# Kernel optimization log

Measured on AMD Instinct MI355X. Metric: run time of the kernel, lower is better.

## Reference

```python
import jax, jax.numpy as jnp
import numpy as np


def setup_inputs() -> dict:
    key = jax.random.key(0)
    ks = jax.random.split(key, 8)
    B, N = 4, 256
    E, C, H = 64, 128, 256
    return {
        "edge_features": jax.random.normal(ks[0], (B, E, N, N), dtype=jnp.float32),
        "node_features": jax.random.normal(ks[1], (B, C, N), dtype=jnp.float32),
        "W1": jax.random.normal(ks[2], (H, E + 2 * C), dtype=jnp.float32) * 0.05,
        "b1": jax.random.normal(ks[3], (H,), dtype=jnp.float32) * 0.05,
        "W2": jax.random.normal(ks[4], (H, H), dtype=jnp.float32) * 0.05,
        "b2": jax.random.normal(ks[5], (H,), dtype=jnp.float32) * 0.05,
        "W3": jax.random.normal(ks[6], (1, H), dtype=jnp.float32) * 0.05,
        "b3": jax.random.normal(ks[7], (1,), dtype=jnp.float32) * 0.05,
    }


def reference(edge_features, node_features, W1, b1, W2, b2, W3, b3):
    B, C, N = node_features.shape
    # node_addon_row: [B, C, N, N] broadcast along last dim; col along dim 2
    row = jnp.broadcast_to(node_features[:, :, :, None], (B, C, N, N))
    col = jnp.broadcast_to(node_features[:, :, None, :], (B, C, N, N))
    x = jnp.concatenate([edge_features, row, col], axis=1)  # [B, E+2C, N, N]
    # 1x1 conv == channel matmul
    x = jax.nn.relu(jnp.einsum('bcnm,oc->bonm', x, W1) + b1[None, :, None, None])
    x = jax.nn.relu(jnp.einsum('bcnm,oc->bonm', x, W2) + b2[None, :, None, None])
    x = jnp.einsum('bcnm,oc->bonm', x, W3) + b3[None, :, None, None]  # [B,1,N,N]
    return x[:, 0, :, :]
```

## Files before the change

kernel.cpp:

```cpp
#include <hip/hip_runtime.h>
#include <stdint.h>

typedef __bf16 bf16x8 __attribute__((ext_vector_type(8)));
typedef __bf16 bf16x4v __attribute__((ext_vector_type(4)));
typedef float  f32x16 __attribute__((ext_vector_type(16)));
typedef float  f32x4t __attribute__((ext_vector_type(4)));
typedef unsigned int u32x2 __attribute__((ext_vector_type(2)));

#define WS_W1S 0
#define WS_W2S 32768
#define WS_R   163840
#define WS_CT  1212416

__global__ __launch_bounds__(256) void prep_all(
    const float* __restrict__ W1, const float* __restrict__ b1,
    const float* __restrict__ W2, const float* __restrict__ node,
    const float* __restrict__ b3, __bf16* __restrict__ w1s,
    __bf16* __restrict__ w2s, float* __restrict__ Rt,
    __bf16* __restrict__ Ctb, float* __restrict__ out) {
    __shared__ float nds[128 * 8];
    const int blk = blockIdx.x;
    if (blk >= 168) {
        float v = b3[0];
        float4 f4 = make_float4(v, v, v, v);
        *(float4*)(out + (blk - 168) * 1024 + threadIdx.x * 4) = f4;
        return;
    }
    if (blk < 40) {
        int t = blk * 256 + threadIdx.x;
        int chunk = t >> 6, lane = t & 63;
        if (chunk < 128) {
            int wid = chunk >> 5, ks = (chunk >> 1) & 15, mb = chunk & 1;
            int o = wid * 64 + mb * 32 + (lane & 31);
            int k = ks * 16 + (lane >> 5) * 8;
            const float* src = W2 + o * 256 + k;
            __bf16* dst = w2s + chunk * 512 + lane * 8;
#pragma unroll
            for (int j = 0; j < 8; ++j) dst[j] = (__bf16)src[j];
        } else if (chunk < 160) {
            int c1 = chunk - 128;
            int wid = c1 >> 3, ks = (c1 >> 1) & 3, mb = c1 & 1;
            int o = wid * 64 + mb * 32 + (lane & 31);
            int k = ks * 16 + (lane >> 5) * 8;
            const float* src = W1 + o * 320 + k;
            __bf16* dst = w1s + c1 * 512 + lane * 8;
#pragma unroll
            for (int j = 0; j < 8; ++j) dst[j] = (__bf16)src[j];
        }
        return;
    }
    const int rcb = blk - 40;
    const int b = rcb >> 5, j0 = (rcb & 31) << 3;
    const int o = threadIdx.x;
    {
        int c = o >> 1, jh = (o & 1) * 4;
        *(float4*)&nds[c * 8 + jh] = *(const float4*)(node + b * 32768 + c * 256 + j0 + jh);
    }
    __syncthreads();
    float aR[8], aC[8];
#pragma unroll
    for (int j = 0; j < 8; ++j) { aR[j] = 0.f; aC[j] = 0.f; }
    const float* wr = W1 + o * 320 + 64;
    const float* wc = W1 + o * 320 + 192;
    for (int c4 = 0; c4 < 32; ++c4) {
        float4 wrv = *(const float4*)(wr + c4 * 4);
        float4 wcv = *(const float4*)(wc + c4 * 4);
        const float* wrp = (const float*)&wrv;
        const float* wcp = (const float*)&wcv;
#pragma unroll
        for (int r = 0; r < 4; ++r) {
            const f32x4t* nrow = (const f32x4t*)&nds[(c4 * 4 + r) * 8];
            f32x4t n0 = nrow[0], n1 = nrow[1];
#pragma unroll
            for (int q = 0; q < 4; ++q) {
                aR[q]     = fmaf(wrp[r], n0[q], aR[q]);
                aR[q + 4] = fmaf(wrp[r], n1[q], aR[q + 4]);
                aC[q]     = fmaf(wcp[r], n0[q], aC[q]);
                aC[q + 4] = fmaf(wcp[r], n1[q], aC[q + 4]);
            }
        }
    }
    float bb = b1[o];
#pragma unroll
    for (int j = 0; j < 8; ++j) {
        int idx = ((b * 256 + j0 + j) << 8) + o;
        Rt[idx] = aR[j] + bb;
        Ctb[idx] = (__bf16)aC[j];
    }
}

__device__ __forceinline__ void lds_barrier() {
    __builtin_amdgcn_sched_barrier(0);
    asm volatile("s_waitcnt lgkmcnt(0)" ::: "memory");
    __builtin_amdgcn_s_barrier();
    __builtin_amdgcn_sched_barrier(0);
}

__global__ __launch_bounds__(512, 2) void fused_main(
    const float* __restrict__ edge, const __bf16* __restrict__ w1s,
    const __bf16* __restrict__ w2s, const float* __restrict__ Rt,
    const __bf16* __restrict__ Ctb, const float* __restrict__ b2,
    const float* __restrict__ W3, const float* __restrict__ b3,
    float* __restrict__ out) {
    __shared__ __bf16 w2lds[32768];
    __shared__ unsigned int lds_e[128 * 34];
    __shared__ unsigned int lds_h1[2][64 * 140];
    __shared__ float lds_c[512];

    const int tid = threadIdx.x;
    const int wid8 = tid >> 6;
    const int og   = wid8 & 3;
    const int rw   = wid8 >> 2;
    const int lane = tid & 63;
    const int p31  = lane & 31;
    const int hi   = lane >> 5;
    const int obase = og << 6;

    const int blk = blockIdx.x;
    const int b   = blk >> 6;
    const int m0  = ((blk >> 4) & 3) << 6;
    const int n0  = (blk & 15) << 4;

    lds_c[tid] = (tid < 256) ? b2[tid] : W3[tid - 256];

    const float4* eg = (const float4*)edge;
    const int tid8 = tid & 255;
    const int a_   = tid8 & 15;
    const int epb  = tid8 >> 4;
    float4 pf[4];

#define PREFETCH(nn)                                                        \
    {                                                                       \
        _Pragma("unroll")                                                   \
        for (int r = 0; r < 2; ++r) {                                       \
            int ep = r * 16 + epb;                                          \
            int f4 = (b * 64 + ep * 2) * 16384 + (nn) * 64 + (m0 >> 2) + a_;\
            pf[r * 2]     = eg[f4];                                         \
            pf[r * 2 + 1] = eg[f4 + 16384];                                 \
        }                                                                   \
    }

#define LOAD_Q(bf, q)                                                       \
    {                                                                       \
        _Pragma("unroll")                                                   \
        for (int ksl = 0; ksl < 4; ++ksl)                                   \
            _Pragma("unroll")                                               \
            for (int mb = 0; mb < 2; ++mb)                                  \
                A2q[bf][ksl][mb] = *(const bf16x8*)(w2_s +                  \
                    ((((og << 4) + (q) * 4 + ksl) << 1) + mb) * 512 + (lane << 3)); \
    }

    PREFETCH(n0 + rw);

    {
        bf16x8 wt[8];
#pragma unroll
        for (int i = 0; i < 8; ++i) {
            int rc = wid8 * 8 + i;
            int mb = rc & 1, k8 = (rc >> 1) & 7, wg = rc >> 4;
            int schunk = (((wg << 4) + 8 + k8) << 1) + mb;
            wt[i] = *(const bf16x8*)(w2s + schunk * 512 + (lane << 3));
        }
#pragma unroll
        for (int i = 0; i < 8; ++i)
            *(bf16x8*)(w2lds + (wid8 * 8 + i) * 512 + (lane << 3)) = wt[i];
    }

    bf16x4v CvR[8][2];
#pragma unroll
    for (int mb = 0; mb < 2; ++mb)
#pragma unroll
        for (int rg = 0; rg < 4; ++rg)
#pragma unroll
            for (int nb = 0; nb < 2; ++nb)
                CvR[mb * 4 + rg][nb] = *(const bf16x4v*)(Ctb +
                    ((b * 256 + m0 + nb * 32 + p31) << 8) + obase + mb * 32 + 8 * rg + 4 * hi);

    bf16x8 A1[2][4];
#pragma unroll
    for (int mb = 0; mb < 2; ++mb)
#pragma unroll
        for (int ks = 0; ks < 4; ++ks)
            A1[mb][ks] = *(const bf16x8*)(w1s +
                ((((og << 2) + ks) << 1) + mb) * 512 + (lane << 3));

    f32x16 acc[2][2];
    bf16x8 A2q[2][4][2];
#pragma unroll 1
    for (int itp = 0; itp < 8; ++itp) {
        const int n_r = n0 + itp * 2 + rw;

        uint64_t w2a = (uint64_t)w2s;
        asm volatile("" : "+s"(w2a));
        const __bf16* w2_s = (const __bf16*)w2a;
        int koff = 0;
        asm volatile("" : "+v"(koff));

#pragma unroll
        for (int r = 0; r < 2; ++r) {
            int ep = r * 16 + epb;
            const float* p0 = (const float*)&pf[r * 2];
            const float* p1 = (const float*)&pf[r * 2 + 1];
#pragma unroll
            for (int i = 0; i < 4; ++i) {
                union { __bf16 h[2]; unsigned int u; } t;
                t.h[0] = (__bf16)p0[i];
                t.h[1] = (__bf16)p1[i];
                lds_e[(rw * 64 + a_ * 4 + i) * 34 + ep] = t.u;
            }
        }
        if (itp < 7) PREFETCH(n0 + (itp + 1) * 2 + rw);

        const int nRow = (b * 256 + n_r) << 8;
        f32x4t Rv[2][4];
#pragma unroll
        for (int mb = 0; mb < 2; ++mb)
#pragma unroll
            for (int rg = 0; rg < 4; ++rg)
                Rv[mb][rg] = *(const f32x4t*)(Rt + nRow + obase + mb * 32 + 8 * rg + 4 * hi);

#pragma unroll
        for (int mb = 0; mb < 2; ++mb)
#pragma unroll
            for (int nb = 0; nb < 2; ++nb)
#pragma unroll
                for (int rg = 0; rg < 4; ++rg)
#pragma unroll
                    for (int rr = 0; rr < 4; ++rr)
                        acc[mb][nb][rg * 4 + rr] = (float)CvR[mb * 4 + rg][nb][rr];

        lds_barrier();

        __builtin_amdgcn_s_setprio(1);
#pragma unroll
        for (int ks = 0; ks < 4; ++ks) {
            bf16x8 B1[2];
#pragma unroll
            for (int nb = 0; nb < 2; ++nb) {
                union { u32x2 d[2]; bf16x8 v; } bb;
                const unsigned int* base = &lds_e[(rw * 64 + nb * 32 + p31) * 34 + ks * 8 + hi * 4];
                bb.d[0] = *(const u32x2*)base;
                bb.d[1] = *(const u32x2*)(base + 2);
                B1[nb] = bb.v;
            }
#pragma unroll
            for (int mb = 0; mb < 2; ++mb) {
                acc[mb][0] = __builtin_amdgcn_mfma_f32_32x32x16_bf16(A1[mb][ks], B1[0], acc[mb][0], 0, 0, 0);
                acc[mb][1] = __builtin_amdgcn_mfma_f32_32x32x16_bf16(A1[mb][ks], B1[1], acc[mb][1], 0, 0, 0);
            }
        }
        __builtin_amdgcn_s_setprio(0);

#pragma unroll
        for (int mb = 0; mb < 2; ++mb) {
#pragma unroll
            for (int rg = 0; rg < 4; ++rg) {
                int och = obase + mb * 32 + 8 * rg + 4 * hi;
                f32x4t Rvv = Rv[mb][rg];
#pragma unroll
                for (int nb = 0; nb < 2; ++nb) {
                    int pix = nb * 32 + p31;
                    union { __bf16 h[4]; u32x2 u; } t;
#pragma unroll
                    for (int rr = 0; rr < 4; ++rr) {
                        float v = acc[mb][nb][rg * 4 + rr] + Rvv[rr];
                        t.h[rr] = (__bf16)fmaxf(v, 0.f);
                    }
                    *(u32x2*)&lds_h1[rw][pix * 140 + (och >> 1)] = t.u;
                }
            }
        }
        LOAD_Q(0, 0);

#pragma unroll
        for (int mb = 0; mb < 2; ++mb)
#pragma unroll
            for (int rg = 0; rg < 4; ++rg) {
                f32x4t b2v = *(const f32x4t*)&lds_c[obase + mb * 32 + 8 * rg + 4 * hi];
#pragma unroll
                for (int nb = 0; nb < 2; ++nb)
#pragma unroll
                    for (int rr = 0; rr < 4; ++rr)
                        acc[mb][nb][rg * 4 + rr] = b2v[rr];
            }

        lds_barrier();

        __builtin_amdgcn_s_setprio(1);
#pragma unroll
        for (int q = 0; q < 2; ++q) {
            if (q == 0) LOAD_Q(1, 1);
#pragma unroll
            for (int ksl = 0; ksl < 4; ++ksl) {
                const int ksg = q * 4 + ksl;
                bf16x8 B2[2];
#pragma unroll
                for (int nb = 0; nb < 2; ++nb)
                    B2[nb] = *(const bf16x8*)&lds_h1[rw][(nb * 32 + p31) * 140 + ksg * 8 + hi * 4];
#pragma unroll
                for (int mb = 0; mb < 2; ++mb) {
                    acc[mb][0] = __builtin_amdgcn_mfma_f32_32x32x16_bf16(A2q[q][ksl][mb], B2[0], acc[mb][0], 0, 0, 0);
                    acc[mb][1] = __builtin_amdgcn_mfma_f32_32x32x16_bf16(A2q[q][ksl][mb], B2[1], acc[mb][1], 0, 0, 0);
                }
            }
        }
#pragma unroll
        for (int k8 = 0; k8 < 8; ++k8) {
            const int ksg = 8 + k8;
            bf16x8 A2r[2];
#pragma unroll
            for (int mb = 0; mb < 2; ++mb)
                A2r[mb] = *(const bf16x8*)(w2lds +
                    (((og * 8 + k8) * 2 + mb) * 512 + koff) + (lane << 3));
            bf16x8 B2[2];
#pragma unroll
            for (int nb = 0; nb < 2; ++nb)
                B2[nb] = *(const bf16x8*)&lds_h1[rw][(nb * 32 + p31) * 140 + ksg * 8 + hi * 4];
#pragma unroll
            for (int mb = 0; mb < 2; ++mb) {
                acc[mb][0] = __builtin_amdgcn_mfma_f32_32x32x16_bf16(A2r[mb], B2[0], acc[mb][0], 0, 0, 0);
                acc[mb][1] = __builtin_amdgcn_mfma_f32_32x32x16_bf16(A2r[mb], B2[1], acc[mb][1], 0, 0, 0);
            }
        }
        __builtin_amdgcn_s_setprio(0);

        float part0 = 0.f, part1 = 0.f;
#pragma unroll
        for (int mb = 0; mb < 2; ++mb) {
#pragma unroll
            for (int rg = 0; rg < 4; ++rg) {
                int och = obase + mb * 32 + 8 * rg + 4 * hi;
                f32x4t w3v = *(const f32x4t*)&lds_c[256 + och];
#pragma unroll
                for (int rr = 0; rr < 4; ++rr) {
                    float h0 = fmaxf(acc[mb][0][rg * 4 + rr], 0.f);
                    float h1v = fmaxf(acc[mb][1][rg * 4 + rr], 0.f);
                    part0 = fmaf(w3v[rr], h0, part0);
                    part1 = fmaf(w3v[rr], h1v, part1);
                }
            }
        }
        part0 += __shfl_xor(part0, 32);
        part1 += __shfl_xor(part1, 32);
        {
            int pix = hi ? (32 + p31) : p31;
            float v = hi ? part1 : part0;
            atomicAdd(&out[((b * 256 + n_r) << 8) + m0 + pix], v);
        }
    }
#undef PREFETCH
#undef LOAD_Q
}

extern "C" void kernel_launch(void* const* d_in, const int* in_sizes, int n_in,
                              void* d_out, int out_size, void* d_ws, size_t ws_size,
                              hipStream_t stream) {
    const float* edge = (const float*)d_in[0];
    const float* node = (const float*)d_in[1];
    const float* W1   = (const float*)d_in[2];
    const float* b1   = (const float*)d_in[3];
    const float* W2   = (const float*)d_in[4];
    const float* b2   = (const float*)d_in[5];
    const float* W3   = (const float*)d_in[6];
    const float* b3   = (const float*)d_in[7];
    char* ws = (char*)d_ws;
    __bf16* w1s = (__bf16*)(ws + WS_W1S);
    __bf16* w2s = (__bf16*)(ws + WS_W2S);
    float*  Rt  = (float*)(ws + WS_R);
    __bf16* Ctb = (__bf16*)(ws + WS_CT);
    float* outp = (float*)d_out;

    prep_all<<<424, 256, 0, stream>>>(W1, b1, W2, node, b3, w1s, w2s, Rt, Ctb, outp);
    fused_main<<<256, 512, 0, stream>>>(edge, w1s, w2s, Rt, Ctb, b2, W3, b3, outp);
}
```

Measured before the change: 146.1 us.

## Warp-specialize fused MLP into layer-1 producer and layer-2 consumer waves

Splits the 8 waves of each block into two roles. Four waves load edge tiles and compute layer 1 into a double-buffered LDS h1 tile. The other four waves hold all of W2 in registers and compute layer 2 plus the W3 reduction for the previous row. This removes the W2 LDS staging, and the per-row layer-2 weight reloads, and lets layer 1 of row s+1 overlap layer 2 of row s. The cost is much higher register pressure in the consumer waves (32 bf16x8 weight fragments) and each MFMA stage now runs on only half the waves, so the speedup depends on how well the two halves balance.

```diff
diff --git a/kernel.cpp b/kernel.cpp
--- a/kernel.cpp
+++ b/kernel.cpp
@@ -102,19 +102,15 @@
     const __bf16* __restrict__ Ctb, const float* __restrict__ b2,
     const float* __restrict__ W3, const float* __restrict__ b3,
     float* __restrict__ out) {
-    __shared__ __bf16 w2lds[32768];
-    __shared__ unsigned int lds_e[128 * 34];
+    __shared__ unsigned int lds_e[2][64 * 34];
     __shared__ unsigned int lds_h1[2][64 * 140];
     __shared__ float lds_c[512];
 
     const int tid = threadIdx.x;
     const int wid8 = tid >> 6;
-    const int og   = wid8 & 3;
-    const int rw   = wid8 >> 2;
     const int lane = tid & 63;
     const int p31  = lane & 31;
     const int hi   = lane >> 5;
-    const int obase = og << 6;
 
     const int blk = blockIdx.x;
     const int b   = blk >> 6;
@@ -123,11 +119,13 @@
 
     lds_c[tid] = (tid < 256) ? b2[tid] : W3[tid - 256];
 
-    const float4* eg = (const float4*)edge;
-    const int tid8 = tid & 255;
-    const int a_   = tid8 & 15;
-    const int epb  = tid8 >> 4;
-    float4 pf[4];
+    if (wid8 < 4) {
+        const int og = wid8;
+        const int obase = og << 6;
+        const float4* eg = (const float4*)edge;
+        const int a_  = tid & 15;
+        const int epb = tid >> 4;
+        float4 pf[4];
 
 #define PREFETCH(nn)                                                        \
     {                                                                       \
@@ -139,217 +137,189 @@
             pf[r * 2 + 1] = eg[f4 + 16384];                                 \
         }                                                                   \
     }
-
-#define LOAD_Q(bf, q)                                                       \
+#define STAGE(bufidx)                                                       \
     {                                                                       \
         _Pragma("unroll")                                                   \
-        for (int ksl = 0; ksl < 4; ++ksl)                                   \
+        for (int r = 0; r < 2; ++r) {                                       \
+            int ep = r * 16 + epb;                                          \
+            const float* p0 = (const float*)&pf[r * 2];                     \
+            const float* p1 = (const float*)&pf[r * 2 + 1];                 \
             _Pragma("unroll")                                               \
-            for (int mb = 0; mb < 2; ++mb)                                  \
-                A2q[bf][ksl][mb] = *(const bf16x8*)(w2_s +                  \
-                    ((((og << 4) + (q) * 4 + ksl) << 1) + mb) * 512 + (lane << 3)); \
-    }
-
-    PREFETCH(n0 + rw);
-
-    {
-        bf16x8 wt[8];
-#pragma unroll
-        for (int i = 0; i < 8; ++i) {
-            int rc = wid8 * 8 + i;
-            int mb = rc & 1, k8 = (rc >> 1) & 7, wg = rc >> 4;
-            int schunk = (((wg << 4) + 8 + k8) << 1) + mb;
-            wt[i] = *(const bf16x8*)(w2s + schunk * 512 + (lane << 3));
+            for (int i = 0; i < 4; ++i) {                                   \
+                union { __bf16 h[2]; unsigned int u; } t;                   \
+                t.h[0] = (__bf16)p0[i];                                     \
+                t.h[1] = (__bf16)p1[i];                                     \
+                lds_e[bufidx][(a_ * 4 + i) * 34 + ep] = t.u;                \
+            }                                                               \
+        }                                                                   \
+    }
+
+        PREFETCH(n0);
+
+        bf16x4v CvR[8][2];
+#pragma unroll
+        for (int mb = 0; mb < 2; ++mb)
+#pragma unroll
+            for (int rg = 0; rg < 4; ++rg)
+#pragma unroll
+                for (int nb = 0; nb < 2; ++nb)
+                    CvR[mb * 4 + rg][nb] = *(const bf16x4v*)(Ctb +
+                        ((b * 256 + m0 + nb * 32 + p31) << 8) + obase + mb * 32 + 8 * rg + 4 * hi);
+
+        bf16x8 A1[2][4];
+#pragma unroll
+        for (int mb = 0; mb < 2; ++mb)
+#pragma unroll
+            for (int ks = 0; ks < 4; ++ks)
+                A1[mb][ks] = *(const bf16x8*)(w1s +
+                    ((((og << 2) + ks) << 1) + mb) * 512 + (lane << 3));
+
+        STAGE(0);
+        PREFETCH(n0 + 1);
+        lds_barrier();
+
+        f32x16 acc[2][2];
+#pragma unroll 1
+        for (int s = 0; s < 16; ++s) {
+            const int buf = s & 1;
+            const int n_r = n0 + s;
+            const int nRow = (b * 256 + n_r) << 8;
+
+            f32x4t Rv[2][4];
+#pragma unroll
+            for (int mb = 0; mb < 2; ++mb)
+#pragma unroll
+                for (int rg = 0; rg < 4; ++rg)
+                    Rv[mb][rg] = *(const f32x4t*)(Rt + nRow + obase + mb * 32 + 8 * rg + 4 * hi);
+
+#pragma unroll
+            for (int mb = 0; mb < 2; ++mb)
+#pragma unroll
+                for (int nb = 0; nb < 2; ++nb)
+#pragma unroll
+                    for (int rg = 0; rg < 4; ++rg)
+#pragma unroll
+                        for (int rr = 0; rr < 4; ++rr)
+                            acc[mb][nb][rg * 4 + rr] = (float)CvR[mb * 4 + rg][nb][rr];
+
+#pragma unroll
+            for (int ks = 0; ks < 4; ++ks) {
+                bf16x8 B1[2];
+#pragma unroll
+                for (int nb = 0; nb < 2; ++nb) {
+                    union { u32x2 d[2]; bf16x8 v; } bb;
+                    const unsigned int* base = &lds_e[buf][(nb * 32 + p31) * 34 + ks * 8 + hi * 4];
+                    bb.d[0] = *(const u32x2*)base;
+                    bb.d[1] = *(const u32x2*)(base + 2);
+                    B1[nb] = bb.v;
+                }
+#pragma unroll
+                for (int mb = 0; mb < 2; ++mb) {
+                    acc[mb][0] = __builtin_amdgcn_mfma_f32_32x32x16_bf16(A1[mb][ks], B1[0], acc[mb][0], 0, 0, 0);
+                    acc[mb][1] = __builtin_amdgcn_mfma_f32_32x32x16_bf16(A1[mb][ks], B1[1], acc[mb][1], 0, 0, 0);
+                }
+            }
+
+#pragma unroll
+            for (int mb = 0; mb < 2; ++mb) {
+#pragma unroll
+                for (int rg = 0; rg < 4; ++rg) {
+                    int och = obase + mb * 32 + 8 * rg + 4 * hi;
+                    f32x4t Rvv = Rv[mb][rg];
+#pragma unroll
+                    for (int nb = 0; nb < 2; ++nb) {
+                        int pix = nb * 32 + p31;
+                        union { __bf16 h[4]; u32x2 u; } t;
+#pragma unroll
+                        for (int rr = 0; rr < 4; ++rr) {
+                            float v = acc[mb][nb][rg * 4 + rr] + Rvv[rr];
+                            t.h[rr] = (__bf16)fmaxf(v, 0.f);
+                        }
+                        *(u32x2*)&lds_h1[buf][pix * 140 + (och >> 1)] = t.u;
+                    }
+                }
+            }
+
+            if (s < 15) STAGE(buf ^ 1);
+            if (s < 14) PREFETCH(n0 + s + 2);
+
+            lds_barrier();
         }
-#pragma unroll
-        for (int i = 0; i < 8; ++i)
-            *(bf16x8*)(w2lds + (wid8 * 8 + i) * 512 + (lane << 3)) = wt[i];
-    }
-
-    bf16x4v CvR[8][2];
-#pragma unroll
-    for (int mb = 0; mb < 2; ++mb)
-#pragma unroll
-        for (int rg = 0; rg < 4; ++rg)
-#pragma unroll
-            for (int nb = 0; nb < 2; ++nb)
-                CvR[mb * 4 + rg][nb] = *(const bf16x4v*)(Ctb +
-                    ((b * 256 + m0 + nb * 32 + p31) << 8) + obase + mb * 32 + 8 * rg + 4 * hi);
-
-    bf16x8 A1[2][4];
-#pragma unroll
-    for (int mb = 0; mb < 2; ++mb)
-#pragma unroll
-        for (int ks = 0; ks < 4; ++ks)
-            A1[mb][ks] = *(const bf16x8*)(w1s +
-                ((((og << 2) + ks) << 1) + mb) * 512 + (lane << 3));
-
-    f32x16 acc[2][2];
-    bf16x8 A2q[2][4][2];
+#undef PREFETCH
+#undef STAGE
+    } else {
+        const int og = wid8 - 4;
+        const int obase = og << 6;
+
+        bf16x8 A2f[16][2];
+#pragma unroll
+        for (int ksg = 0; ksg < 16; ++ksg)
+#pragma unroll
+            for (int mb = 0; mb < 2; ++mb)
+                A2f[ksg][mb] = *(const bf16x8*)(w2s +
+                    ((((og << 4) + ksg) << 1) + mb) * 512 + (lane << 3));
+
+        lds_barrier();
+
+        f32x16 acc[2][2];
 #pragma unroll 1
-    for (int itp = 0; itp < 8; ++itp) {
-        const int n_r = n0 + itp * 2 + rw;
-
-        uint64_t w2a = (uint64_t)w2s;
-        asm volatile("" : "+s"(w2a));
-        const __bf16* w2_s = (const __bf16*)w2a;
-        int koff = 0;
-        asm volatile("" : "+v"(koff));
-
-#pragma unroll
-        for (int r = 0; r < 2; ++r) {
-            int ep = r * 16 + epb;
-            const float* p0 = (const float*)&pf[r * 2];
-            const float* p1 = (const float*)&pf[r * 2 + 1];
-#pragma unroll
-            for (int i = 0; i < 4; ++i) {
-                union { __bf16 h[2]; unsigned int u; } t;
-                t.h[0] = (__bf16)p0[i];
-                t.h[1] = (__bf16)p1[i];
-                lds_e[(rw * 64 + a_ * 4 + i) * 34 + ep] = t.u;
+        for (int s = 0; s < 16; ++s) {
+            lds_barrier();
+            const int buf = s & 1;
+            const int n_r = n0 + s;
+
+#pragma unroll
+            for (int mb = 0; mb < 2; ++mb)
+#pragma unroll
+                for (int rg = 0; rg < 4; ++rg) {
+                    f32x4t b2v = *(const f32x4t*)&lds_c[obase + mb * 32 + 8 * rg + 4 * hi];
+#pragma unroll
+                    for (int nb = 0; nb < 2; ++nb)
+#pragma unroll
+                        for (int rr = 0; rr < 4; ++rr)
+                            acc[mb][nb][rg * 4 + rr] = b2v[rr];
+                }
+
+            __builtin_amdgcn_s_setprio(1);
+#pragma unroll
+            for (int ksg = 0; ksg < 16; ++ksg) {
+                bf16x8 B2[2];
+#pragma unroll
+                for (int nb = 0; nb < 2; ++nb)
+                    B2[nb] = *(const bf16x8*)&lds_h1[buf][(nb * 32 + p31) * 140 + ksg * 8 + hi * 4];
+#pragma unroll
+                for (int mb = 0; mb < 2; ++mb) {
+                    acc[mb][0] = __builtin_amdgcn_mfma_f32_32x32x16_bf16(A2f[ksg][mb], B2[0], acc[mb][0], 0, 0, 0);
+                    acc[mb][1] = __builtin_amdgcn_mfma_f32_32x32x16_bf16(A2f[ksg][mb], B2[1], acc[mb][1], 0, 0, 0);
+                }
+            }
+            __builtin_amdgcn_s_setprio(0);
+
+            float part0 = 0.f, part1 = 0.f;
+#pragma unroll
+            for (int mb = 0; mb < 2; ++mb) {
+#pragma unroll
+                for (int rg = 0; rg < 4; ++rg) {
+                    int och = obase + mb * 32 + 8 * rg + 4 * hi;
+                    f32x4t w3v = *(const f32x4t*)&lds_c[256 + och];
+#pragma unroll
+                    for (int rr = 0; rr < 4; ++rr) {
+                        float h0 = fmaxf(acc[mb][0][rg * 4 + rr], 0.f);
+                        float h1v = fmaxf(acc[mb][1][rg * 4 + rr], 0.f);
+                        part0 = fmaf(w3v[rr], h0, part0);
+                        part1 = fmaf(w3v[rr], h1v, part1);
+                    }
+                }
+            }
+            part0 += __shfl_xor(part0, 32);
+            part1 += __shfl_xor(part1, 32);
+            {
+                int pix = hi ? (32 + p31) : p31;
+                float v = hi ? part1 : part0;
+                atomicAdd(&out[((b * 256 + n_r) << 8) + m0 + pix], v);
             }
         }
-        if (itp < 7) PREFETCH(n0 + (itp + 1) * 2 + rw);
-
-        const int nRow = (b * 256 + n_r) << 8;
-        f32x4t Rv[2][4];
-#pragma unroll
-        for (int mb = 0; mb < 2; ++mb)
-#pragma unroll
-            for (int rg = 0; rg < 4; ++rg)
-                Rv[mb][rg] = *(const f32x4t*)(Rt + nRow + obase + mb * 32 + 8 * rg + 4 * hi);
-
-#pragma unroll
-        for (int mb = 0; mb < 2; ++mb)
-#pragma unroll
-            for (int nb = 0; nb < 2; ++nb)
-#pragma unroll
-                for (int rg = 0; rg < 4; ++rg)
-#pragma unroll
-                    for (int rr = 0; rr < 4; ++rr)
-                        acc[mb][nb][rg * 4 + rr] = (float)CvR[mb * 4 + rg][nb][rr];
-
-        lds_barrier();
-
-        __builtin_amdgcn_s_setprio(1);
-#pragma unroll
-        for (int ks = 0; ks < 4; ++ks) {
-            bf16x8 B1[2];
-#pragma unroll
-            for (int nb = 0; nb < 2; ++nb) {
-                union { u32x2 d[2]; bf16x8 v; } bb;
-                const unsigned int* base = &lds_e[(rw * 64 + nb * 32 + p31) * 34 + ks * 8 + hi * 4];
-                bb.d[0] = *(const u32x2*)base;
-                bb.d[1] = *(const u32x2*)(base + 2);
-                B1[nb] = bb.v;
-            }
-#pragma unroll
-            for (int mb = 0; mb < 2; ++mb) {
-                acc[mb][0] = __builtin_amdgcn_mfma_f32_32x32x16_bf16(A1[mb][ks], B1[0], acc[mb][0], 0, 0, 0);
-                acc[mb][1] = __builtin_amdgcn_mfma_f32_32x32x16_bf16(A1[mb][ks], B1[1], acc[mb][1], 0, 0, 0);
-            }
-        }
-        __builtin_amdgcn_s_setprio(0);
-
-#pragma unroll
-        for (int mb = 0; mb < 2; ++mb) {
-#pragma unroll
-            for (int rg = 0; rg < 4; ++rg) {
-                int och = obase + mb * 32 + 8 * rg + 4 * hi;
-                f32x4t Rvv = Rv[mb][rg];
-#pragma unroll
-                for (int nb = 0; nb < 2; ++nb) {
-                    int pix = nb * 32 + p31;
-                    union { __bf16 h[4]; u32x2 u; } t;
-#pragma unroll
-                    for (int rr = 0; rr < 4; ++rr) {
-                        float v = acc[mb][nb][rg * 4 + rr] + Rvv[rr];
-                        t.h[rr] = (__bf16)fmaxf(v, 0.f);
-                    }
-                    *(u32x2*)&lds_h1[rw][pix * 140 + (och >> 1)] = t.u;
-                }
-            }
-        }
-        LOAD_Q(0, 0);
-
-#pragma unroll
-        for (int mb = 0; mb < 2; ++mb)
-#pragma unroll
-            for (int rg = 0; rg < 4; ++rg) {
-                f32x4t b2v = *(const f32x4t*)&lds_c[obase + mb * 32 + 8 * rg + 4 * hi];
-#pragma unroll
-                for (int nb = 0; nb < 2; ++nb)
-#pragma unroll
-                    for (int rr = 0; rr < 4; ++rr)
-                        acc[mb][nb][rg * 4 + rr] = b2v[rr];
-            }
-
-        lds_barrier();
-
-        __builtin_amdgcn_s_setprio(1);
-#pragma unroll
-        for (int q = 0; q < 2; ++q) {
-            if (q == 0) LOAD_Q(1, 1);
-#pragma unroll
-            for (int ksl = 0; ksl < 4; ++ksl) {
-                const int ksg = q * 4 + ksl;
-                bf16x8 B2[2];
-#pragma unroll
-                for (int nb = 0; nb < 2; ++nb)
-                    B2[nb] = *(const bf16x8*)&lds_h1[rw][(nb * 32 + p31) * 140 + ksg * 8 + hi * 4];
-#pragma unroll
-                for (int mb = 0; mb < 2; ++mb) {
-                    acc[mb][0] = __builtin_amdgcn_mfma_f32_32x32x16_bf16(A2q[q][ksl][mb], B2[0], acc[mb][0], 0, 0, 0);
-                    acc[mb][1] = __builtin_amdgcn_mfma_f32_32x32x16_bf16(A2q[q][ksl][mb], B2[1], acc[mb][1], 0, 0, 0);
-                }
-            }
-        }
-#pragma unroll
-        for (int k8 = 0; k8 < 8; ++k8) {
-            const int ksg = 8 + k8;
-            bf16x8 A2r[2];
-#pragma unroll
-            for (int mb = 0; mb < 2; ++mb)
-                A2r[mb] = *(const bf16x8*)(w2lds +
-                    (((og * 8 + k8) * 2 + mb) * 512 + koff) + (lane << 3));
-            bf16x8 B2[2];
-#pragma unroll
-            for (int nb = 0; nb < 2; ++nb)
-                B2[nb] = *(const bf16x8*)&lds_h1[rw][(nb * 32 + p31) * 140 + ksg * 8 + hi * 4];
-#pragma unroll
-            for (int mb = 0; mb < 2; ++mb) {
-                acc[mb][0] = __builtin_amdgcn_mfma_f32_32x32x16_bf16(A2r[mb], B2[0], acc[mb][0], 0, 0, 0);
-                acc[mb][1] = __builtin_amdgcn_mfma_f32_32x32x16_bf16(A2r[mb], B2[1], acc[mb][1], 0, 0, 0);
-            }
-        }
-        __builtin_amdgcn_s_setprio(0);
-
-        float part0 = 0.f, part1 = 0.f;
-#pragma unroll
-        for (int mb = 0; mb < 2; ++mb) {
-#pragma unroll
-            for (int rg = 0; rg < 4; ++rg) {
-                int och = obase + mb * 32 + 8 * rg + 4 * hi;
-                f32x4t w3v = *(const f32x4t*)&lds_c[256 + och];
-#pragma unroll
-                for (int rr = 0; rr < 4; ++rr) {
-                    float h0 = fmaxf(acc[mb][0][rg * 4 + rr], 0.f);
-                    float h1v = fmaxf(acc[mb][1][rg * 4 + rr], 0.f);
-                    part0 = fmaf(w3v[rr], h0, part0);
-                    part1 = fmaf(w3v[rr], h1v, part1);
-                }
-            }
-        }
-        part0 += __shfl_xor(part0, 32);
-        part1 += __shfl_xor(part1, 32);
-        {
-            int pix = hi ? (32 + p31) : p31;
-            float v = hi ? part1 : part0;
-            atomicAdd(&out[((b * 256 + n_r) << 8) + m0 + pix], v);
-        }
-    }
-#undef PREFETCH
-#undef LOAD_Q
+    }
 }
 
 extern "C" void kernel_launch(void* const* d_in, const int* in_sizes, int n_in,
```

Measured after the change: 141.4 us. 1.03x faster.
